# Kernel optimization log

Hardware: AMD Instinct MI355X
Metric: run time of the kernel (lower is better)

The kernel has to match this reference:

```python
import jax, jax.numpy as jnp
import numpy as np
from jax import lax

B, C, H, W = 4, 24, 128, 128
R = 7
NUM_CLASSES = 6
MAX_STEPS = 8


def _conv(x, w, b, pad):
    y = lax.conv_general_dilated(x, w, (1, 1), [(pad, pad), (pad, pad)],
                                 dimension_numbers=("NCHW", "OIHW", "NCHW"))
    return y + b[None, :, None, None]


def setup_inputs() -> dict:
    key = jax.random.key(0)
    ks = jax.random.split(key, 16)
    s = 0.05
    inp = {
        "depth_latent": jax.random.normal(ks[0], (B, C, H, W), jnp.float32),
        "texture_features": jax.random.normal(ks[1], (B, 3, H, W), jnp.float32),
        "class_labels": jax.random.randint(ks[2], (B,), 0, NUM_CLASSES),
        # texture_encoder
        "w_te1": jax.random.normal(ks[3], (64, 3, 3, 3), jnp.float32) * s,
        "b_te1": jnp.zeros((64,), jnp.float32),
        "w_te2": jax.random.normal(ks[4], (128, 64, 3, 3), jnp.float32) * s,
        "b_te2": jnp.zeros((128,), jnp.float32),
        # class embedding [num_classes, 128]
        "emb": jax.random.normal(ks[5], (NUM_CLASSES, 128), jnp.float32) * s,
        # fusion_layer: Conv2d(256,256,3) -> Conv2d(256, C*R*R, 1)
        "w_f1": jax.random.normal(ks[6], (256, 256, 3, 3), jnp.float32) * s,
        "b_f1": jnp.zeros((256,), jnp.float32),
        "w_f2": jax.random.normal(ks[7], (C * R * R, 256, 1, 1), jnp.float32) * s,
        "b_f2": jnp.zeros((C * R * R,), jnp.float32),
        # class_gate: Conv2d(128,64,3) -> Conv2d(64,num_classes,1)
        "w_g1": jax.random.normal(ks[8], (64, 128, 3, 3), jnp.float32) * s,
        "b_g1": jnp.zeros((64,), jnp.float32),
        "w_g2": jax.random.normal(ks[9], (NUM_CLASSES, 64, 1, 1), jnp.float32) * s,
        "b_g2": jnp.zeros((NUM_CLASSES,), jnp.float32),
        "class_intensity": jnp.ones((1, NUM_CLASSES, 1, 1), jnp.float32),
    }
    return inp


def _forward(depth_latent, texture_features, class_labels,
             w_te1, b_te1, w_te2, b_te2, emb,
             w_f1, b_f1, w_f2, b_f2,
             w_g1, b_g1, w_g2, b_g2, class_intensity):
    pad = R // 2
    # texture encoder
    tex = jax.nn.relu(_conv(texture_features, w_te1, b_te1, 1))
    tex = jax.nn.relu(_conv(tex, w_te2, b_te2, 1))  # [B,128,H,W]

    # 1-D integer class label path
    class_cond = jax.nn.one_hot(class_labels, NUM_CLASSES, dtype=jnp.float32)[:, :, None, None]  # [B,K,1,1]
    class_emb = emb[class_labels][:, :, None, None]  # [B,128,1,1]

    gate = jax.nn.sigmoid(_conv(jax.nn.relu(_conv(tex, w_g1, b_g1, 1)), w_g2, b_g2, 0))
    class_gate = gate * class_cond  # [B,K,H,W]

    fused = jnp.concatenate([tex, jnp.broadcast_to(class_emb, (tex.shape[0], 128, H, W))], axis=1)
    weights = _conv(jax.nn.relu(_conv(fused, w_f1, b_f1, 1)), w_f2, b_f2, 0)
    weights = weights.reshape(-1, C, R * R, H, W)

    intensity_map = (class_gate * class_intensity).sum(axis=1, keepdims=True)  # [B,1,H,W]
    weights = weights * intensity_map[:, :, None]  # [B,C,R*R,H,W]
    weights = jax.nn.softmax(weights, axis=2)

    def diffusion_step(lat):
        p = jnp.pad(lat, ((0, 0), (0, 0), (pad, pad), (pad, pad)), mode="edge")
        # unfold order: kernel row-major (i*R + j)
        windows = jnp.stack([p[:, :, i:i + H, j:j + W]
                             for i in range(R) for j in range(R)], axis=2)
        return (windows * weights).sum(axis=2)

    enhanced = lax.fori_loop(0, MAX_STEPS, lambda _, lat: diffusion_step(lat), depth_latent)

    condition_map = intensity_map * class_gate.sum(axis=1, keepdims=True)
    return enhanced, class_gate, condition_map


def reference(depth_latent, texture_features, class_labels,
              w_te1, b_te1, w_te2, b_te2, emb,
              w_f1, b_f1, w_f2, b_f2,
              w_g1, b_g1, w_g2, b_g2, class_intensity):
    return _forward(depth_latent, texture_features, class_labels,
                    w_te1, b_te1, w_te2, b_te2, emb,
                    w_f1, b_f1, w_f2, b_f2,
                    w_g1, b_g1, w_g2, b_g2, class_intensity)
```

## Files before the change

### kernel.cpp

```cpp
#include <hip/hip_runtime.h>
#include <hip/hip_bf16.h>
#include <stdint.h>

#define DINL __device__ __forceinline__

DINL float bf2f(__hip_bfloat16 v) { return __bfloat162float(v); }
DINL __hip_bfloat16 f2bf(float v) { return __float2bfloat16(v); }
DINL float bflo(unsigned int u) { return __uint_as_float(u << 16); }
DINL float bfhi(unsigned int u) { return __uint_as_float(u & 0xffff0000u); }

DINL float loadf(float v) { return v; }
DINL float loadf(__hip_bfloat16 v) { return __bfloat162float(v); }

typedef __attribute__((ext_vector_type(8))) short bf16x8;
typedef __attribute__((ext_vector_type(4))) float f32x4;

#define O_WTE1 0
#define O_WG2  1792
#define O_SS   2304
#define O_INT  11520
#define BO_W2B   308224u
#define BO_TE2B 1094656u
#define BO_WG1B 1242112u
#define BO_WF1B 1389568u
#define BO_TEX  4194304u
#define BO_F1   20971520u
#define BO_PING 54525952u
#define BO_PONG 60817408u
#define BO_W    67108864u
#define BO_T1   BO_W
#define BO_G1   (BO_W + 16777216u)

__global__ __launch_bounds__(256) void prep_kernel(
    const float* __restrict__ w_te1, const float* __restrict__ w_te2,
    const float* __restrict__ w_g1,  const float* __restrict__ w_f1,
    const float* __restrict__ w_f2,  const float* __restrict__ w_g2,
    const float* __restrict__ emb,   const int* __restrict__ labels,
    float* __restrict__ wsf)
{
  const int gid = blockIdx.x * 256 + threadIdx.x;
  const int stride = gridDim.x * 256;
  const int A0 = 1728, A1 = A0 + 393216, A2 = A1 + 73728, A3 = A2 + 73728,
            A4 = A3 + 294912, A5 = A4 + 384;
  __hip_bfloat16* w2b  = (__hip_bfloat16*)((char*)wsf + BO_W2B);
  __hip_bfloat16* te2b = (__hip_bfloat16*)((char*)wsf + BO_TE2B);
  __hip_bfloat16* g1b  = (__hip_bfloat16*)((char*)wsf + BO_WG1B);
  __hip_bfloat16* f1b  = (__hip_bfloat16*)((char*)wsf + BO_WF1B);
  for (int i = gid; i < A5; i += stride) {
    if (i < A0) {
      int s = i; int o = s / 27; int r = s - o * 27; int ic = r / 9; int t = r - ic * 9;
      wsf[O_WTE1 + (((o >> 5) * 3 + ic) * 9 + t) * 32 + (o & 31)] = w_te1[s];
    } else if (i < A1) {
      int s = i - A0;
      int j = s & 7; int lane = (s >> 3) & 63; int ks = (s >> 9) & 7;
      int mt = (s >> 12) & 3; int c = s >> 14;
      int tap = mt * 16 + (lane & 15);
      int k = ks * 32 + (lane >> 4) * 8 + j;
      float v = (tap < 49) ? w_f2[(c * 49 + tap) * 256 + k] : 0.f;
      w2b[s] = f2bf(v);
    } else if (i < A2) {
      int s = i - A1;
      int k = s & 31; int n = (s >> 5) & 63; int u = s >> 11;
      int t = u % 9; int v = u / 9; int kc = v & 1; int ocg = v >> 1;
      te2b[s] = f2bf(w_te2[((ocg * 64 + n) * 64 + kc * 32 + k) * 9 + t]);
    } else if (i < A3) {
      int s = i - A2;
      int k = s & 31; int n = (s >> 5) & 63; int u = s >> 11;
      int t = u % 9; int kc = u / 9;
      g1b[s] = f2bf(w_g1[(n * 128 + kc * 32 + k) * 9 + t]);
    } else if (i < A4) {
      int s = i - A3;
      int k = s & 31; int n = (s >> 5) & 63; int u = s >> 11;
      int t = u % 9; int v = u / 9; int kc = v & 3; int ocg = v >> 2;
      f1b[s] = f2bf(w_f1[((ocg * 64 + n) * 256 + kc * 32 + k) * 9 + t]);
    } else {
      int s = i - A4;
      wsf[O_WG2 + s] = w_g2[s];
    }
  }
  if (gid < 16384) {
    const int g = gid >> 4, slot = gid & 15;
    const int b = g >> 8, o = g & 255;
    const int lab = labels[b];
    float St[9];
#pragma unroll
    for (int t = 0; t < 9; ++t) St[t] = 0.f;
#pragma unroll 2
    for (int k = 0; k < 8; ++k) {
      const int i = slot * 8 + k;
      const float e = emb[lab * 128 + i];
      const float* wr = w_f1 + (size_t)(o * 256 + 128 + i) * 9;
#pragma unroll
      for (int t = 0; t < 9; ++t) St[t] += wr[t] * e;
    }
#pragma unroll
    for (int d = 1; d < 16; d <<= 1)
#pragma unroll
      for (int t = 0; t < 9; ++t) St[t] += __shfl_xor(St[t], d, 64);
    if (slot == 0) {
#pragma unroll
      for (int ch = 0; ch < 3; ++ch)
#pragma unroll
        for (int cw = 0; cw < 3; ++cw) {
          float sum = 0.f;
#pragma unroll
          for (int t = 0; t < 9; ++t) {
            int kh = t / 3, kw = t - kh * 3;
            bool ok = !(ch == 0 && kh == 0) && !(ch == 2 && kh == 2) &&
                      !(cw == 0 && kw == 0) && !(cw == 2 && kw == 2);
            if (ok) sum += St[t];
          }
          wsf[O_SS + g * 9 + ch * 3 + cw] = sum;
        }
    }
  }
}

template<typename TIn, int ICH, bool PIXMAJOR>
__global__ __launch_bounds__(256, 2) void conv3x3_kernel(
    const TIn* __restrict__ in, const float* __restrict__ wf,
    const float* __restrict__ bias,
    __hip_bfloat16* __restrict__ out, const int och_total)
{
  constexpr int CH = (ICH < 16) ? ICH : 16;
  constexpr int NCHUNK = ICH / CH;
  __shared__ TIn sIn[CH][18][20];
  const int tid = threadIdx.x;
  const int b = blockIdx.z;
  const int ob = blockIdx.y;
  const int och0 = ob * 32;
  const int tileY = blockIdx.x >> 3, tileX = blockIdx.x & 7;
  const int ty = tid >> 4, tx = tid & 15;
  const int h = tileY * 16 + ty, w = tileX * 16 + tx;
  const int h0 = tileY * 16 - 1, w0 = tileX * 16 - 1;

  float acc[32];
#pragma unroll
  for (int o = 0; o < 32; ++o) acc[o] = bias[och0 + o];

  for (int cc = 0; cc < NCHUNK; ++cc) {
    if (cc) __syncthreads();
    for (int e = tid; e < CH * 324; e += 256) {
      int ic = e / 324, r = e - ic * 324;
      int y = r / 18, x = r - y * 18;
      int gh = h0 + y, gw = w0 + x;
      TIn v = TIn(0.f);
      if ((unsigned)gh < 128u && (unsigned)gw < 128u)
        v = in[((b * ICH + cc * CH + ic) << 14) + (gh << 7) + gw];
      sIn[ic][y][x] = v;
    }
    __syncthreads();
#pragma unroll 1
    for (int ic = 0; ic < CH; ++ic) {
      const float* wrow = wf + (ob * ICH + cc * CH + ic) * 288;
#pragma unroll
      for (int t = 0; t < 9; ++t) {
        const int kh = t / 3, kw = t - kh * 3;
        const float v = loadf(sIn[ic][ty + kh][tx + kw]);
#pragma unroll
        for (int o = 0; o < 32; ++o)
          acc[o] = fmaf(wrow[t * 32 + o], v, acc[o]);
      }
    }
  }

  const int pix = (h << 7) + w;
  if constexpr (!PIXMAJOR) {
#pragma unroll
    for (int o = 0; o < 32; ++o)
      out[((b * och_total + och0 + o) << 14) + pix] = f2bf(fmaxf(acc[o], 0.f));
  } else {
    union { uint4 u4[4]; __hip_bfloat16 hh[32]; } pk;
#pragma unroll
    for (int o = 0; o < 32; ++o) pk.hh[o] = f2bf(fmaxf(acc[o], 0.f));
    uint4* dst = reinterpret_cast<uint4*>(out + ((size_t)(b << 14) + pix) * och_total + och0);
#pragma unroll
    for (int i = 0; i < 4; ++i) dst[i] = pk.u4[i];
  }
}

template<int ICH, bool ADD_SS>
__global__ __launch_bounds__(256, 2) void conv3x3_mfma_kernel(
    const __hip_bfloat16* __restrict__ in, const __hip_bfloat16* __restrict__ wb,
    const float* __restrict__ bias, const float* __restrict__ SS,
    __hip_bfloat16* __restrict__ out, const int och_total)
{
  constexpr int NKC = ICH / 32;
  __shared__ __hip_bfloat16 sH[324][40];
  __shared__ __hip_bfloat16 sW[9][64][40];
  const int tid = threadIdx.x, b = blockIdx.z, ocg = blockIdx.y;
  const int tileY = blockIdx.x >> 3, tileX = blockIdx.x & 7;
  const int h0 = tileY * 16 - 1, w0 = tileX * 16 - 1;
  const int wave = tid >> 6, lane = tid & 63, m16 = lane & 15, quad = lane >> 4;

  f32x4 acc[4][4];
#pragma unroll
  for (int i = 0; i < 4; ++i)
#pragma unroll
    for (int j = 0; j < 4; ++j) acc[i][j] = f32x4{0.f, 0.f, 0.f, 0.f};

  for (int kc = 0; kc < NKC; ++kc) {
    if (kc) __syncthreads();
    for (int e = tid; e < 1296; e += 256) {
      int pos = e >> 2, q = e & 3;
      int y = pos / 18, x = pos - y * 18;
      int gh = h0 + y, gw = w0 + x;
      uint4 v = uint4{0u, 0u, 0u, 0u};
      if ((unsigned)gh < 128u && (unsigned)gw < 128u)
        v = *(const uint4*)(in + ((size_t)((b << 14) + (gh << 7) + gw)) * ICH + kc * 32 + q * 8);
      *(uint4*)&sH[pos][q * 8] = v;
    }
    const uint4* wsrc = (const uint4*)(wb + ((size_t)(ocg * NKC + kc)) * 9 * 64 * 32);
    for (int e = tid; e < 2304; e += 256) {
      int q = e & 3, n = (e >> 2) & 63, t = e >> 8;
      *(uint4*)&sW[t][n][q * 8] = wsrc[e];
    }
    __syncthreads();
#pragma unroll
    for (int t = 0; t < 9; ++t) {
      const int dy = t / 3, dx = t - dy * 3;
      bf16x8 bfr[4];
#pragma unroll
      for (int nt = 0; nt < 4; ++nt)
        bfr[nt] = *(const bf16x8*)&sW[t][nt * 16 + m16][quad * 8];
#pragma unroll
      for (int mi = 0; mi < 4; ++mi) {
        const int py = wave * 4 + mi;
        const bf16x8 afr = *(const bf16x8*)&sH[(py + dy) * 18 + dx + m16][quad * 8];
#pragma unroll
        for (int nt = 0; nt < 4; ++nt)
          acc[mi][nt] = __builtin_amdgcn_mfma_f32_16x16x32_bf16(afr, bfr[nt], acc[mi][nt], 0, 0, 0);
      }
    }
  }

  float bv[4];
#pragma unroll
  for (int nt = 0; nt < 4; ++nt) bv[nt] = bias[ocg * 64 + nt * 16 + m16];
#pragma unroll
  for (int mi = 0; mi < 4; ++mi) {
    const int py = wave * 4 + mi;
    const int h = tileY * 16 + py;
    const int chc = (h == 0) ? 0 : ((h == 127) ? 2 : 1);
#pragma unroll
    for (int nt = 0; nt < 4; ++nt) {
      float sr0 = 0.f, sr1 = 0.f, sr2 = 0.f;
      if constexpr (ADD_SS) {
        const float* sp = SS + ((size_t)(b << 8) + (ocg * 64 + nt * 16 + m16)) * 9;
        sr0 = sp[chc * 3 + 0]; sr1 = sp[chc * 3 + 1]; sr2 = sp[chc * 3 + 2];
      }
      const int och = ocg * 64 + nt * 16 + m16;
#pragma unroll
      for (int r = 0; r < 4; ++r) {
        const int px = quad * 4 + r;
        const int w = tileX * 16 + px;
        float v = acc[mi][nt][r] + bv[nt];
        if constexpr (ADD_SS)
          v += (w == 0) ? sr0 : ((w == 127) ? sr2 : sr1);
        v = fmaxf(v, 0.f);
        out[((size_t)((b << 14) + (h << 7) + w)) * och_total + och] = f2bf(v);
      }
    }
  }
}

__global__ __launch_bounds__(256) void gate2_kernel(
    const __hip_bfloat16* __restrict__ g1, const float* __restrict__ wg2,
    const float* __restrict__ b_g2, const int* __restrict__ labels,
    const float* __restrict__ ci,
    float* __restrict__ out_cg, float* __restrict__ out_cond,
    float* __restrict__ inten)
{
  const int b = blockIdx.y;
  const int pix = blockIdx.x * 256 + threadIdx.x;
  float acc[6];
#pragma unroll
  for (int k = 0; k < 6; ++k) acc[k] = b_g2[k];
  const uint4* gp = (const uint4*)(g1 + ((size_t)((b << 14) + pix)) * 64);
#pragma unroll
  for (int i4 = 0; i4 < 8; ++i4) {
    const uint4 q = gp[i4];
    const float v0 = bflo(q.x), v1 = bfhi(q.x), v2 = bflo(q.y), v3 = bfhi(q.y);
    const float v4 = bflo(q.z), v5 = bfhi(q.z), v6 = bflo(q.w), v7 = bfhi(q.w);
#pragma unroll
    for (int k = 0; k < 6; ++k) {
      const float* wr = wg2 + k * 64 + i4 * 8;
      acc[k] = fmaf(wr[0], v0, acc[k]); acc[k] = fmaf(wr[1], v1, acc[k]);
      acc[k] = fmaf(wr[2], v2, acc[k]); acc[k] = fmaf(wr[3], v3, acc[k]);
      acc[k] = fmaf(wr[4], v4, acc[k]); acc[k] = fmaf(wr[5], v5, acc[k]);
      acc[k] = fmaf(wr[6], v6, acc[k]); acc[k] = fmaf(wr[7], v7, acc[k]);
    }
  }
  const int lab = labels[b];
  float gate[6], gl = 0.f;
#pragma unroll
  for (int k = 0; k < 6; ++k) {
    gate[k] = 1.f / (1.f + __expf(-acc[k]));
    gl = (k == lab) ? gate[k] : gl;
  }
  const float civ = ci[lab];
  const float it = gl * civ;
#pragma unroll
  for (int k = 0; k < 6; ++k)
    out_cg[((b * 6 + k) << 14) + pix] = (k == lab) ? gate[k] : 0.f;
  inten[(b << 14) + pix] = it;
  out_cond[(b << 14) + pix] = it * gl;
}

__global__ __launch_bounds__(256, 3) void gemm_softmax_kernel(
    const __hip_bfloat16* __restrict__ f1, const __hip_bfloat16* __restrict__ w2b,
    const float* __restrict__ b_f2, const float* __restrict__ inten,
    __hip_bfloat16* __restrict__ wout)
{
  __shared__ __hip_bfloat16 sW[2][8192];
  __shared__ __hip_bfloat16 sT[49][136];
  const int tid = threadIdx.x;
  const int pix0 = blockIdx.x * 128;
  const int c0 = blockIdx.y * 8;
  const int wave = tid >> 6, lane = tid & 63;
  const int n16 = lane & 15, quad = lane >> 4;
  const int p0 = pix0 + wave * 16 + n16;
  const int p1 = p0 + 64;

  bf16x8 bfr0[8], bfr1[8];
#pragma unroll
  for (int ks = 0; ks < 8; ++ks) {
    bfr0[ks] = *(const bf16x8*)(f1 + (size_t)p0 * 256 + ks * 32 + quad * 8);
    bfr1[ks] = *(const bf16x8*)(f1 + (size_t)p1 * 256 + ks * 32 + quad * 8);
  }

  const float s0v = inten[p0], s1v = inten[p1];
  const int ob = pix0 >> 14, op = pix0 & 16383;

#define W2U(u) ((const uint4*)(w2b + ((((size_t)c0 + ((u) >> 1)) * 4 + (((u) & 1) << 1)) << 12)))

  {
    const uint4* s0 = W2U(0);
    uint4 t0[4];
#pragma unroll
    for (int j = 0; j < 4; ++j) t0[j] = s0[tid + j * 256];
    uint4* d0 = (uint4*)&sW[0][0];
#pragma unroll
    for (int j = 0; j < 4; ++j) d0[tid + j * 256] = t0[j];
  }
  __syncthreads();

#pragma unroll 1
  for (int cl = 0; cl < 8; ++cl) {
    const int c = c0 + cl;
    f32x4 ac0[4], ac1[4];
#pragma unroll
    for (int mt = 0; mt < 4; ++mt) { ac0[mt] = f32x4{0.f,0.f,0.f,0.f}; ac1[mt] = f32x4{0.f,0.f,0.f,0.f}; }

#pragma unroll
    for (int h = 0; h < 2; ++h) {
      const int u = cl * 2 + h;
      const uint4* sn = W2U(u < 15 ? u + 1 : 15);
      uint4 tn[4];
#pragma unroll
      for (int j = 0; j < 4; ++j) tn[j] = sn[tid + j * 256];

      const __hip_bfloat16* bufp = &sW[u & 1][0];
#pragma unroll
      for (int ks = 0; ks < 8; ++ks) {
        const bf16x8 a0 = *(const bf16x8*)(bufp + ((ks) * 64 + lane) * 8);
        const bf16x8 a1 = *(const bf16x8*)(bufp + ((8 + ks) * 64 + lane) * 8);
        ac0[h * 2 + 0] = __builtin_amdgcn_mfma_f32_16x16x32_bf16(a0, bfr0[ks], ac0[h * 2 + 0], 0, 0, 0);
        ac1[h * 2 + 0] = __builtin_amdgcn_mfma_f32_16x16x32_bf16(a0, bfr1[ks], ac1[h * 2 + 0], 0, 0, 0);
        ac0[h * 2 + 1] = __builtin_amdgcn_mfma_f32_16x16x32_bf16(a1, bfr0[ks], ac0[h * 2 + 1], 0, 0, 0);
        ac1[h * 2 + 1] = __builtin_amdgcn_mfma_f32_16x16x32_bf16(a1, bfr1[ks], ac1[h * 2 + 1], 0, 0, 0);
      }

      uint4* dn = (uint4*)&sW[(u + 1) & 1][0];
#pragma unroll
      for (int j = 0; j < 4; ++j) dn[tid + j * 256] = tn[j];
      __syncthreads();
    }

#pragma unroll
    for (int g = 0; g < 2; ++g) {
      f32x4* ac = g ? ac1 : ac0;
      const float s = g ? s1v : s0v;
      float mx = -3.4e38f;
#pragma unroll
      for (int mt = 0; mt < 4; ++mt)
#pragma unroll
        for (int r = 0; r < 4; ++r) {
          const int tap = mt * 16 + quad * 4 + r;
          const bool ok = tap < 49;
          const float lv = ok ? (ac[mt][r] + b_f2[c * 49 + (ok ? tap : 0)]) * s : -3.4e38f;
          ac[mt][r] = lv;
          mx = fmaxf(mx, lv);
        }
      mx = fmaxf(mx, __shfl_xor(mx, 16, 64));
      mx = fmaxf(mx, __shfl_xor(mx, 32, 64));
      float sum = 0.f;
#pragma unroll
      for (int mt = 0; mt < 4; ++mt)
#pragma unroll
        for (int r = 0; r < 4; ++r) {
          const float e = __expf(ac[mt][r] - mx);
          ac[mt][r] = e;
          sum += e;
        }
      sum += __shfl_xor(sum, 16, 64);
      sum += __shfl_xor(sum, 32, 64);
      const float rs = 1.f / sum;

      const int px = wave * 16 + n16 + g * 64;
#pragma unroll
      for (int mt = 0; mt < 4; ++mt)
#pragma unroll
        for (int r = 0; r < 4; ++r) {
          const int tap = mt * 16 + quad * 4 + r;
          if (tap < 49) sT[tap][px] = f2bf(ac[mt][r] * rs);
        }
    }
    __syncthreads();

    __hip_bfloat16* wob = wout + (((size_t)(ob * 24 + c) * 49) << 14) + op;
    for (int e = tid; e < 784; e += 256) {
      const int tap = e >> 4, qq = e & 15;
      *(uint4*)(wob + ((size_t)tap << 14) + qq * 8) = *(const uint4*)&sT[tap][qq * 8];
    }
  }
#undef W2U
}

__global__ __launch_bounds__(256) void diff_kernel(
    const float* __restrict__ lin, const __hip_bfloat16* __restrict__ wts,
    float* __restrict__ lout)
{
  __shared__ float sT[14][136];
  const int bc = blockIdx.y;
  const int h0 = blockIdx.x * 8;
  const int tid = threadIdx.x;
  for (int e = tid; e < 14 * 134; e += 256) {
    int y = e / 134, x = e - y * 134;
    int gh = min(max(h0 - 3 + y, 0), 127), gw = min(max(x - 3, 0), 127);
    sT[y][x] = lin[(bc << 14) + (gh << 7) + gw];
  }
  __syncthreads();
  const int tw = (tid & 31) * 4;
  const int ty = tid >> 5;
  const int h = h0 + ty;
  const __hip_bfloat16* wp = wts + (((size_t)bc * 49) << 14) + (h << 7) + tw;
  float a0 = 0.f, a1 = 0.f, a2 = 0.f, a3 = 0.f;
#pragma unroll
  for (int kh = 0; kh < 7; ++kh) {
    const float* row = &sT[ty + kh][tw];
    float r[12];
    *(f32x4*)&r[0] = *(const f32x4*)(row);
    *(f32x4*)&r[4] = *(const f32x4*)(row + 4);
    *(f32x4*)&r[8] = *(const f32x4*)(row + 8);
#pragma unroll
    for (int kw = 0; kw < 7; ++kw) {
      const int t = kh * 7 + kw;
      const uint2 wq = *(const uint2*)(wp + ((size_t)t << 14));
      a0 = fmaf(bflo(wq.x), r[kw],     a0);
      a1 = fmaf(bfhi(wq.x), r[kw + 1], a1);
      a2 = fmaf(bflo(wq.y), r[kw + 2], a2);
      a3 = fmaf(bfhi(wq.y), r[kw + 3], a3);
    }
  }
  *(f32x4*)(lout + (bc << 14) + (h << 7) + tw) = f32x4{a0, a1, a2, a3};
}

extern "C" void kernel_launch(void* const* d_in, const int* in_sizes, int n_in,
                              void* d_out, int out_size, void* d_ws, size_t ws_size,
                              hipStream_t stream)
{
  const float* depth = (const float*)d_in[0];
  const float* texf  = (const float*)d_in[1];
  const int*   labels= (const int*)d_in[2];
  const float* w_te1 = (const float*)d_in[3];
  const float* b_te1 = (const float*)d_in[4];
  const float* w_te2 = (const float*)d_in[5];
  const float* b_te2 = (const float*)d_in[6];
  const float* emb   = (const float*)d_in[7];
  const float* w_f1  = (const float*)d_in[8];
  const float* b_f1  = (const float*)d_in[9];
  const float* w_f2  = (const float*)d_in[10];
  const float* b_f2  = (const float*)d_in[11];
  const float* w_g1  = (const float*)d_in[12];
  const float* b_g1  = (const float*)d_in[13];
  const float* w_g2  = (const float*)d_in[14];
  const float* b_g2  = (const float*)d_in[15];
  const float* ci    = (const float*)d_in[16];

  char*  ws  = (char*)d_ws;
  float* wsf = (float*)d_ws;
  __hip_bfloat16* w2bf  = (__hip_bfloat16*)(ws + BO_W2B);
  __hip_bfloat16* te2bf = (__hip_bfloat16*)(ws + BO_TE2B);
  __hip_bfloat16* g1bf  = (__hip_bfloat16*)(ws + BO_WG1B);
  __hip_bfloat16* f1bf  = (__hip_bfloat16*)(ws + BO_WF1B);
  __hip_bfloat16* tex   = (__hip_bfloat16*)(ws + BO_TEX);
  __hip_bfloat16* f1    = (__hip_bfloat16*)(ws + BO_F1);
  float* ping           = (float*)(ws + BO_PING);
  float* pong           = (float*)(ws + BO_PONG);
  __hip_bfloat16* wts   = (__hip_bfloat16*)(ws + BO_W);
  __hip_bfloat16* t1    = (__hip_bfloat16*)(ws + BO_T1);
  __hip_bfloat16* g1    = (__hip_bfloat16*)(ws + BO_G1);

  float* out      = (float*)d_out;
  float* out_enh  = out;
  float* out_cg   = out + 1572864;
  float* out_cond = out + 1966080;

  prep_kernel<<<512, 256, 0, stream>>>(w_te1, w_te2, w_g1, w_f1, w_f2, w_g2, emb, labels, wsf);
  conv3x3_kernel<float, 3, true><<<dim3(64, 2, 4), 256, 0, stream>>>(texf, wsf + O_WTE1, b_te1, t1, 64);
  conv3x3_mfma_kernel<64,  false><<<dim3(64, 2, 4), 256, 0, stream>>>(t1,  te2bf, b_te2, nullptr,      tex, 128);
  conv3x3_mfma_kernel<128, false><<<dim3(64, 1, 4), 256, 0, stream>>>(tex, g1bf,  b_g1,  nullptr,      g1,  64);
  gate2_kernel<<<dim3(64, 4), 256, 0, stream>>>(g1, wsf + O_WG2, b_g2, labels, ci, out_cg, out_cond, wsf + O_INT);
  conv3x3_mfma_kernel<128, true ><<<dim3(64, 4, 4), 256, 0, stream>>>(tex, f1bf,  b_f1,  wsf + O_SS,   f1,  256);
  gemm_softmax_kernel<<<dim3(512, 3), 256, 0, stream>>>(f1, w2bf, b_f2, wsf + O_INT, wts);

  dim3 dgrid(16, 96);
  diff_kernel<<<dgrid, 256, 0, stream>>>(depth, wts, ping);
  diff_kernel<<<dgrid, 256, 0, stream>>>(ping, wts, pong);
  diff_kernel<<<dgrid, 256, 0, stream>>>(pong, wts, ping);
  diff_kernel<<<dgrid, 256, 0, stream>>>(ping, wts, pong);
  diff_kernel<<<dgrid, 256, 0, stream>>>(pong, wts, ping);
  diff_kernel<<<dgrid, 256, 0, stream>>>(ping, wts, pong);
  diff_kernel<<<dgrid, 256, 0, stream>>>(pong, wts, ping);
  diff_kernel<<<dgrid, 256, 0, stream>>>(ping, wts, out_enh);
}
```

Measured before the change: 493.2 us.

## Fuse class-gate 1x1 conv into gate conv epilogue; use direct global-to-LDS loads

Folds the former gate2 kernel into the epilogue of the 128->64 gate conv. The ReLU'd conv output is staged through shared memory and the 6-class 1x1 conv, sigmoid and intensity outputs are computed per pixel, so the g1 intermediate no longer makes a global round trip and one launch is gone. Separately, the weight double-buffer in gemm_softmax now uses global_load_lds to copy straight into LDS instead of going through registers, cutting VGPR pressure and register-to-LDS stores. Shared memory is merged into one flat array so the gate epilogue can reuse it. This adds an extra sync and the async LDS load pattern relies on the existing barrier for ordering.

Result: no change. 490.4 us (-0.6%).

```diff
diff --git a/kernel.cpp b/kernel.cpp
--- a/kernel.cpp
+++ b/kernel.cpp
@@ -14,6 +14,12 @@
 
 typedef __attribute__((ext_vector_type(8))) short bf16x8;
 typedef __attribute__((ext_vector_type(4))) float f32x4;
+
+DINL void gld_lds16(const void* g, void* l) {
+  __builtin_amdgcn_global_load_lds(
+      (const __attribute__((address_space(1))) unsigned int*)g,
+      (__attribute__((address_space(3))) unsigned int*)l, 16, 0, 0);
+}
 
 #define O_WTE1 0
 #define O_WG2  1792
@@ -29,7 +35,6 @@
 #define BO_PONG 60817408u
 #define BO_W    67108864u
 #define BO_T1   BO_W
-#define BO_G1   (BO_W + 16777216u)
 
 __global__ __launch_bounds__(256) void prep_kernel(
     const float* __restrict__ w_te1, const float* __restrict__ w_te2,
@@ -179,15 +184,20 @@
   }
 }
 
-template<int ICH, bool ADD_SS>
+template<int ICH, bool ADD_SS, bool GATE>
 __global__ __launch_bounds__(256, 2) void conv3x3_mfma_kernel(
     const __hip_bfloat16* __restrict__ in, const __hip_bfloat16* __restrict__ wb,
     const float* __restrict__ bias, const float* __restrict__ SS,
-    __hip_bfloat16* __restrict__ out, const int och_total)
+    __hip_bfloat16* __restrict__ out, const int och_total,
+    const float* __restrict__ wg2, const float* __restrict__ b_g2,
+    const int* __restrict__ labels, const float* __restrict__ ci,
+    float* __restrict__ out_cg, float* __restrict__ out_cond,
+    float* __restrict__ inten)
 {
   constexpr int NKC = ICH / 32;
-  __shared__ __hip_bfloat16 sH[324][40];
-  __shared__ __hip_bfloat16 sW[9][64][40];
+  __shared__ __hip_bfloat16 smem[36000];
+#define SHX(pos, k) smem[(pos) * 40 + (k)]
+#define SWX(t, n, k) smem[12960 + (((t) * 64 + (n)) * 40) + (k)]
   const int tid = threadIdx.x, b = blockIdx.z, ocg = blockIdx.y;
   const int tileY = blockIdx.x >> 3, tileX = blockIdx.x & 7;
   const int h0 = tileY * 16 - 1, w0 = tileX * 16 - 1;
@@ -208,12 +218,12 @@
       uint4 v = uint4{0u, 0u, 0u, 0u};
       if ((unsigned)gh < 128u && (unsigned)gw < 128u)
         v = *(const uint4*)(in + ((size_t)((b << 14) + (gh << 7) + gw)) * ICH + kc * 32 + q * 8);
-      *(uint4*)&sH[pos][q * 8] = v;
+      *(uint4*)&SHX(pos, q * 8) = v;
     }
     const uint4* wsrc = (const uint4*)(wb + ((size_t)(ocg * NKC + kc)) * 9 * 64 * 32);
     for (int e = tid; e < 2304; e += 256) {
       int q = e & 3, n = (e >> 2) & 63, t = e >> 8;
-      *(uint4*)&sW[t][n][q * 8] = wsrc[e];
+      *(uint4*)&SWX(t, n, q * 8) = wsrc[e];
     }
     __syncthreads();
 #pragma unroll
@@ -222,11 +232,11 @@
       bf16x8 bfr[4];
 #pragma unroll
       for (int nt = 0; nt < 4; ++nt)
-        bfr[nt] = *(const bf16x8*)&sW[t][nt * 16 + m16][quad * 8];
+        bfr[nt] = *(const bf16x8*)&SWX(t, nt * 16 + m16, quad * 8);
 #pragma unroll
       for (int mi = 0; mi < 4; ++mi) {
         const int py = wave * 4 + mi;
-        const bf16x8 afr = *(const bf16x8*)&sH[(py + dy) * 18 + dx + m16][quad * 8];
+        const bf16x8 afr = *(const bf16x8*)&SHX((py + dy) * 18 + dx + m16, quad * 8);
 #pragma unroll
         for (int nt = 0; nt < 4; ++nt)
           acc[mi][nt] = __builtin_amdgcn_mfma_f32_16x16x32_bf16(afr, bfr[nt], acc[mi][nt], 0, 0, 0);
@@ -237,6 +247,56 @@
   float bv[4];
 #pragma unroll
   for (int nt = 0; nt < 4; ++nt) bv[nt] = bias[ocg * 64 + nt * 16 + m16];
+
+  if constexpr (GATE) {
+    __syncthreads();
+    __hip_bfloat16* sG = smem;
+#pragma unroll
+    for (int mi = 0; mi < 4; ++mi)
+#pragma unroll
+      for (int nt = 0; nt < 4; ++nt) {
+        const int och = nt * 16 + m16;
+#pragma unroll
+        for (int r = 0; r < 4; ++r) {
+          const int p = (wave * 4 + mi) * 16 + quad * 4 + r;
+          sG[p * 68 + och] = f2bf(fmaxf(acc[mi][nt][r] + bv[nt], 0.f));
+        }
+      }
+    __syncthreads();
+    const int p = tid;
+    float a6[6];
+#pragma unroll
+    for (int k = 0; k < 6; ++k) a6[k] = b_g2[k];
+#pragma unroll
+    for (int i8 = 0; i8 < 8; ++i8) {
+      const bf16x8 v8 = *(const bf16x8*)&sG[p * 68 + i8 * 8];
+#pragma unroll
+      for (int j = 0; j < 8; ++j) {
+        const float v = bf2f(((const __hip_bfloat16*)&v8)[j]);
+#pragma unroll
+        for (int k = 0; k < 6; ++k)
+          a6[k] = fmaf(wg2[k * 64 + i8 * 8 + j], v, a6[k]);
+      }
+    }
+    const int lab = labels[b];
+    float gate[6], gl = 0.f;
+#pragma unroll
+    for (int k = 0; k < 6; ++k) {
+      gate[k] = 1.f / (1.f + __expf(-a6[k]));
+      gl = (k == lab) ? gate[k] : gl;
+    }
+    const float civ = ci[lab];
+    const float it = gl * civ;
+    const int h = tileY * 16 + (p >> 4), w = tileX * 16 + (p & 15);
+    const int pix = (h << 7) + w;
+#pragma unroll
+    for (int k = 0; k < 6; ++k)
+      out_cg[((b * 6 + k) << 14) + pix] = (k == lab) ? gate[k] : 0.f;
+    inten[(b << 14) + pix] = it;
+    out_cond[(b << 14) + pix] = it * gl;
+    return;
+  }
+
 #pragma unroll
   for (int mi = 0; mi < 4; ++mi) {
     const int py = wave * 4 + mi;
@@ -262,49 +322,8 @@
       }
     }
   }
-}
-
-__global__ __launch_bounds__(256) void gate2_kernel(
-    const __hip_bfloat16* __restrict__ g1, const float* __restrict__ wg2,
-    const float* __restrict__ b_g2, const int* __restrict__ labels,
-    const float* __restrict__ ci,
-    float* __restrict__ out_cg, float* __restrict__ out_cond,
-    float* __restrict__ inten)
-{
-  const int b = blockIdx.y;
-  const int pix = blockIdx.x * 256 + threadIdx.x;
-  float acc[6];
-#pragma unroll
-  for (int k = 0; k < 6; ++k) acc[k] = b_g2[k];
-  const uint4* gp = (const uint4*)(g1 + ((size_t)((b << 14) + pix)) * 64);
-#pragma unroll
-  for (int i4 = 0; i4 < 8; ++i4) {
-    const uint4 q = gp[i4];
-    const float v0 = bflo(q.x), v1 = bfhi(q.x), v2 = bflo(q.y), v3 = bfhi(q.y);
-    const float v4 = bflo(q.z), v5 = bfhi(q.z), v6 = bflo(q.w), v7 = bfhi(q.w);
-#pragma unroll
-    for (int k = 0; k < 6; ++k) {
-      const float* wr = wg2 + k * 64 + i4 * 8;
-      acc[k] = fmaf(wr[0], v0, acc[k]); acc[k] = fmaf(wr[1], v1, acc[k]);
-      acc[k] = fmaf(wr[2], v2, acc[k]); acc[k] = fmaf(wr[3], v3, acc[k]);
-      acc[k] = fmaf(wr[4], v4, acc[k]); acc[k] = fmaf(wr[5], v5, acc[k]);
-      acc[k] = fmaf(wr[6], v6, acc[k]); acc[k] = fmaf(wr[7], v7, acc[k]);
-    }
-  }
-  const int lab = labels[b];
-  float gate[6], gl = 0.f;
-#pragma unroll
-  for (int k = 0; k < 6; ++k) {
-    gate[k] = 1.f / (1.f + __expf(-acc[k]));
-    gl = (k == lab) ? gate[k] : gl;
-  }
-  const float civ = ci[lab];
-  const float it = gl * civ;
-#pragma unroll
-  for (int k = 0; k < 6; ++k)
-    out_cg[((b * 6 + k) << 14) + pix] = (k == lab) ? gate[k] : 0.f;
-  inten[(b << 14) + pix] = it;
-  out_cond[(b << 14) + pix] = it * gl;
+#undef SHX
+#undef SWX
 }
 
 __global__ __launch_bounds__(256, 3) void gemm_softmax_kernel(
@@ -336,12 +355,10 @@
 
   {
     const uint4* s0 = W2U(0);
-    uint4 t0[4];
-#pragma unroll
-    for (int j = 0; j < 4; ++j) t0[j] = s0[tid + j * 256];
     uint4* d0 = (uint4*)&sW[0][0];
 #pragma unroll
-    for (int j = 0; j < 4; ++j) d0[tid + j * 256] = t0[j];
+    for (int j = 0; j < 4; ++j)
+      gld_lds16(s0 + tid + j * 256, d0 + tid + j * 256);
   }
   __syncthreads();
 
@@ -355,10 +372,13 @@
 #pragma unroll
     for (int h = 0; h < 2; ++h) {
       const int u = cl * 2 + h;
-      const uint4* sn = W2U(u < 15 ? u + 1 : 15);
-      uint4 tn[4];
-#pragma unroll
-      for (int j = 0; j < 4; ++j) tn[j] = sn[tid + j * 256];
+      {
+        const uint4* sn = W2U(u < 15 ? u + 1 : 15);
+        uint4* dn = (uint4*)&sW[(u + 1) & 1][0];
+#pragma unroll
+        for (int j = 0; j < 4; ++j)
+          gld_lds16(sn + tid + j * 256, dn + tid + j * 256);
+      }
 
       const __hip_bfloat16* bufp = &sW[u & 1][0];
 #pragma unroll
@@ -370,10 +390,6 @@
         ac0[h * 2 + 1] = __builtin_amdgcn_mfma_f32_16x16x32_bf16(a1, bfr0[ks], ac0[h * 2 + 1], 0, 0, 0);
         ac1[h * 2 + 1] = __builtin_amdgcn_mfma_f32_16x16x32_bf16(a1, bfr1[ks], ac1[h * 2 + 1], 0, 0, 0);
       }
-
-      uint4* dn = (uint4*)&sW[(u + 1) & 1][0];
-#pragma unroll
-      for (int j = 0; j < 4; ++j) dn[tid + j * 256] = tn[j];
       __syncthreads();
     }
 
@@ -500,7 +516,6 @@
   float* pong           = (float*)(ws + BO_PONG);
   __hip_bfloat16* wts   = (__hip_bfloat16*)(ws + BO_W);
   __hip_bfloat16* t1    = (__hip_bfloat16*)(ws + BO_T1);
-  __hip_bfloat16* g1    = (__hip_bfloat16*)(ws + BO_G1);
 
   float* out      = (float*)d_out;
   float* out_enh  = out;
@@ -509,10 +524,15 @@
 
   prep_kernel<<<512, 256, 0, stream>>>(w_te1, w_te2, w_g1, w_f1, w_f2, w_g2, emb, labels, wsf);
   conv3x3_kernel<float, 3, true><<<dim3(64, 2, 4), 256, 0, stream>>>(texf, wsf + O_WTE1, b_te1, t1, 64);
-  conv3x3_mfma_kernel<64,  false><<<dim3(64, 2, 4), 256, 0, stream>>>(t1,  te2bf, b_te2, nullptr,      tex, 128);
-  conv3x3_mfma_kernel<128, false><<<dim3(64, 1, 4), 256, 0, stream>>>(tex, g1bf,  b_g1,  nullptr,      g1,  64);
-  gate2_kernel<<<dim3(64, 4), 256, 0, stream>>>(g1, wsf + O_WG2, b_g2, labels, ci, out_cg, out_cond, wsf + O_INT);
-  conv3x3_mfma_kernel<128, true ><<<dim3(64, 4, 4), 256, 0, stream>>>(tex, f1bf,  b_f1,  wsf + O_SS,   f1,  256);
+  conv3x3_mfma_kernel<64,  false, false><<<dim3(64, 2, 4), 256, 0, stream>>>(
+      t1, te2bf, b_te2, nullptr, tex, 128,
+      nullptr, nullptr, nullptr, nullptr, nullptr, nullptr, nullptr);
+  conv3x3_mfma_kernel<128, false, true><<<dim3(64, 1, 4), 256, 0, stream>>>(
+      tex, g1bf, b_g1, nullptr, nullptr, 64,
+      wsf + O_WG2, b_g2, labels, ci, out_cg, out_cond, wsf + O_INT);
+  conv3x3_mfma_kernel<128, true, false><<<dim3(64, 4, 4), 256, 0, stream>>>(
+      tex, f1bf, b_f1, wsf + O_SS, f1, 256,
+      nullptr, nullptr, nullptr, nullptr, nullptr, nullptr, nullptr);
   gemm_softmax_kernel<<<dim3(512, 3), 256, 0, stream>>>(f1, w2bf, b_f2, wsf + O_INT, wts);
 
   dim3 dgrid(16, 96);
```
